# Optimization experiments

Measured on AMD Instinct MI355X. Metric: run time of the kernel, lower is better.

## Reference

```python
import jax, jax.numpy as jnp
import numpy as np

N, E, CIN, H, HEADS, B = 50000, 800000, 16, 64, 3, 64
D0 = HEADS * H            # conv1 out (heads concatenated) = 192
D1 = D0 + CIN             # x1 dim = 208
D2 = 2 * D1               # x2 dim = 416
MLP_IN = 3 * D2           # 1248
MLP_HID = MLP_IN // 2     # 624
EPS = 1e-5


def setup_inputs() -> dict:
    key = jax.random.key(0)
    ks = jax.random.split(key, 24)
    r = lambda k, s, sc=0.05: (jax.random.normal(k, s, dtype=jnp.float32) * sc)
    inp = {
        'x': jax.random.normal(ks[0], (N, CIN), dtype=jnp.float32),
        'edge_index': jax.random.randint(ks[1], (2, E), 0, N, dtype=jnp.int32),
        'edge_attr': jax.random.normal(ks[2], (E, 4), dtype=jnp.float32),
        'batch': jnp.sort(jax.random.randint(ks[3], (N,), 0, B, dtype=jnp.int32)),
        # conv1 (GeneralConv, heads=3, concat): msg/edge/self linears -> D0
        'W_msg1': r(ks[4], (CIN, D0)), 'b_msg1': jnp.zeros((D0,), jnp.float32),
        'W_edge1': r(ks[5], (4, D0)), 'b_edge1': jnp.zeros((D0,), jnp.float32),
        'W_self1': r(ks[6], (CIN, D0)), 'b_self1': jnp.zeros((D0,), jnp.float32),
        'g1': jnp.ones((D0,), jnp.float32), 'be1': jnp.zeros((D0,), jnp.float32),
        # conv2 (GeneralConv, heads=1, in==out -> identity self)
        'W_msg2': r(ks[7], (D1, D1)), 'b_msg2': jnp.zeros((D1,), jnp.float32),
        'W_edge2': r(ks[8], (4, D1)), 'b_edge2': jnp.zeros((D1,), jnp.float32),
        'g2': jnp.ones((D1,), jnp.float32), 'be2': jnp.zeros((D1,), jnp.float32),
        # MLP head
        'W_l1': r(ks[9], (MLP_IN, MLP_HID)), 'b_l1': jnp.zeros((MLP_HID,), jnp.float32),
        'alpha': jnp.asarray(0.25, jnp.float32),  # PReLU default
        'W_l2': r(ks[10], (MLP_HID, 2)), 'b_l2': jnp.zeros((2,), jnp.float32),
    }
    return inp


def _bn(h, g, b):
    m = h.mean(axis=0)
    v = h.var(axis=0)  # biased, like torch BatchNorm training mode
    return (h - m) * jax.lax.rsqrt(v + EPS) * g + b


def reference(x, edge_index, edge_attr, batch,
              W_msg1, b_msg1, W_edge1, b_edge1, W_self1, b_self1, g1, be1,
              W_msg2, b_msg2, W_edge2, b_edge2, g2, be2,
              W_l1, b_l1, alpha, W_l2, b_l2):
    src, dst = edge_index[0], edge_index[1]
    # conv1: gather -> linear msg + edge feature -> scatter-add -> + self linear
    m1 = x[src] @ W_msg1 + b_msg1 + edge_attr @ W_edge1 + b_edge1   # [E, D0]
    h1 = jax.ops.segment_sum(m1, dst, num_segments=N) + (x @ W_self1 + b_self1)
    h1 = _bn(h1, g1, be1)
    x1 = jnp.concatenate([h1, x], axis=1)                           # [N, D1]
    # conv2 (identity self-connection since in==out)
    m2 = x1[src] @ W_msg2 + b_msg2 + edge_attr @ W_edge2 + b_edge2  # [E, D1]
    h2 = jax.ops.segment_sum(m2, dst, num_segments=N) + x1
    h2 = _bn(h2, g2, be2)
    x2 = jnp.concatenate([h2, x1], axis=1)                          # [N, D2]
    # global add / mean / max pooling by graph id
    s = jax.ops.segment_sum(x2, batch, num_segments=B)
    cnt = jax.ops.segment_sum(jnp.ones((x2.shape[0], 1), x2.dtype), batch, num_segments=B)
    mean = s / jnp.maximum(cnt, 1.0)
    mx = jax.ops.segment_max(x2, batch, num_segments=B)
    pooled = jnp.concatenate([s, mx, mean], axis=1)                 # [B, 3*D2]
    # MLP head: Linear -> Dropout(0) -> PReLU -> Linear -> log_softmax
    h = pooled @ W_l1 + b_l1
    h = jnp.where(h >= 0, h, alpha * h)
    logits = h @ W_l2 + b_l2
    return jax.nn.log_softmax(logits, axis=-1)
```

## Files before the change

kernel.cpp:

```cpp
#include <hip/hip_runtime.h>

typedef __attribute__((ext_vector_type(8))) short short8;
typedef __attribute__((ext_vector_type(4))) float f32x4;
typedef unsigned short u16;
typedef unsigned int u32;

__device__ __forceinline__ u16 f2bf(float f) {
  u32 u = __float_as_uint(f);
  u = (u + 0x7fffu + ((u >> 16) & 1u)) >> 16;
  return (u16)u;
}
__device__ __forceinline__ float bf2f(u16 v) { return __uint_as_float((u32)v << 16); }
__device__ __forceinline__ void atomAddF(float* p, float v) { unsafeAtomicAdd(p, v); }
__device__ __forceinline__ void addp(float* v, u32 p) {
  v[0] += bf2f((u16)p);
  v[1] += bf2f((u16)(p >> 16));
}

__global__ void prep_k(const float* __restrict__ Wm1, const float* __restrict__ We1,
                       const float* __restrict__ Ws1, const float* __restrict__ Wm2,
                       const float* __restrict__ Wl1, const float* __restrict__ x,
                       const int* __restrict__ batch, u16* __restrict__ Wp1,
                       u16* __restrict__ Wp2, u16* __restrict__ Wp3,
                       u16* __restrict__ xbf, int* __restrict__ gstart,
                       int* __restrict__ gend, int* __restrict__ deg,
                       float* __restrict__ bns1p, float* __restrict__ bns2p, int N, int E) {
  int tid = blockIdx.x * 256 + threadIdx.x;
  if (tid < 64 * 192) {
    int k = tid / 192, n = tid % 192;
    float v = 0.f;
    if (k < 16) v = Wm1[k * 192 + n];
    else if (k < 20) v = We1[(k - 16) * 192 + n];
    else if (k < 36) v = Ws1[(k - 20) * 192 + n];
    Wp1[((k >> 3) * 192 + n) * 8 + (k & 7)] = f2bf(v);
  }
  if (tid < 224 * 208) {
    int k = tid / 208, n = tid % 208;
    float v = (k < 208) ? Wm2[k * 208 + n] : 0.f;
    Wp2[((k >> 3) * 208 + n) * 8 + (k & 7)] = f2bf(v);
  }
  if (tid < N * 8) {
    float2 p = *(const float2*)(x + (size_t)tid * 2);
    *(u32*)(xbf + (size_t)tid * 2) = (u32)f2bf(p.x) | ((u32)f2bf(p.y) << 16);
  }
  if (tid < N) {
    int b = batch[tid];
    if (tid == 0 || batch[tid - 1] != b) gstart[b] = tid;
    if (tid == N - 1 || batch[tid + 1] != b) gend[b] = tid;
    deg[tid] = 0;
  }
  if (tid < 64 * 384) bns1p[tid] = 0.f;
  if (tid < 64 * 832) bns2p[tid] = 0.f;
  if (tid < 1248 * 624) {
    int k = tid / 624, n = tid % 624;
    Wp3[((size_t)(k >> 3) * 624 + n) * 8 + (k & 7)] = f2bf(Wl1[(size_t)k * 624 + n]);
  }
}

__global__ void count_k(const int* __restrict__ ei, int* __restrict__ deg,
                        int* __restrict__ ord, int E) {
  int e = blockIdx.x * 256 + threadIdx.x;
  if (e >= E) return;
  ord[e] = atomicAdd(&deg[ei[E + e]], 1);
}

__global__ void scanA_k(const int* __restrict__ deg, int* __restrict__ bsum, int N) {
  __shared__ int sh[256];
  int t = threadIdx.x;
  int i = blockIdx.x * 256 + t;
  sh[t] = (i < N) ? deg[i] : 0;
  __syncthreads();
  for (int off = 128; off > 0; off >>= 1) {
    if (t < off) sh[t] += sh[t + off];
    __syncthreads();
  }
  if (t == 0) bsum[blockIdx.x] = sh[0];
}

__global__ void scanC_k(const int* __restrict__ deg, const int* __restrict__ bsum,
                        int* __restrict__ rowptr, int N, int nb) {
  __shared__ int sb2[256];
  __shared__ int sh[256];
  int t = threadIdx.x;
  int bv = (t < nb) ? bsum[t] : 0;
  sb2[t] = bv;
  __syncthreads();
  for (int off = 1; off < 256; off <<= 1) {
    int u = (t >= off) ? sb2[t - off] : 0;
    __syncthreads();
    sb2[t] += u;
    __syncthreads();
  }
  int bpref = (blockIdx.x == 0) ? 0 : sb2[blockIdx.x - 1];
  int i = blockIdx.x * 256 + t;
  int d = (i < N) ? deg[i] : 0;
  sh[t] = d;
  __syncthreads();
  for (int off = 1; off < 256; off <<= 1) {
    int u = (t >= off) ? sh[t - off] : 0;
    __syncthreads();
    sh[t] += u;
    __syncthreads();
  }
  int excl = sh[t] - d + bpref;
  if (i < N) {
    rowptr[i] = excl;
    if (i == N - 1) rowptr[N] = excl + d;
  }
}

__global__ void scatter_k(const int* __restrict__ ei, const float* __restrict__ ea,
                          const int* __restrict__ ord, const int* __restrict__ rowptr,
                          int4* __restrict__ se16, int E) {
  int e = blockIdx.x * 256 + threadIdx.x;
  if (e >= E) return;
  int s = ei[e], d = ei[E + e];
  float4 w = *(const float4*)(ea + (size_t)e * 4);
  int slot = rowptr[d] + ord[e];
  int4 ent;
  ent.x = s;
  ent.y = (int)((u32)f2bf(w.x) | ((u32)f2bf(w.y) << 16));
  ent.z = (int)((u32)f2bf(w.z) | ((u32)f2bf(w.w) << 16));
  ent.w = 0;
  se16[slot] = ent;
}

__global__ void __launch_bounds__(256) conv1_k(
    const int4* __restrict__ se16, const int* __restrict__ rowptr,
    const u16* __restrict__ xbf, const u16* __restrict__ Bp,
    const float* __restrict__ bm1, const float* __restrict__ be1,
    const float* __restrict__ bs1, u16* __restrict__ acc1c, u16* __restrict__ h1bf,
    float* __restrict__ bns1p, int N) {
  __shared__ __align__(16) u16 Uls[16][72];
  __shared__ float degls[16];
  int tid = threadIdx.x;
  int nl = tid >> 4, q = tid & 15;
  int n = blockIdx.x * 16 + nl;
  bool nval = n < N;
  int j0 = nval ? rowptr[n] : 0;
  int j1 = nval ? rowptr[n + 1] : 0;
  float v[20];
#pragma unroll
  for (int i = 0; i < 20; ++i) v[i] = 0.f;
  for (int j = j0 + q; j < j1; j += 16) {
    int4 p = se16[j];
    const uint4* xs = (const uint4*)(xbf + (size_t)p.x * 16);
    uint4 x0 = xs[0], x1 = xs[1];
    addp(v + 0, x0.x); addp(v + 2, x0.y); addp(v + 4, x0.z); addp(v + 6, x0.w);
    addp(v + 8, x1.x); addp(v + 10, x1.y); addp(v + 12, x1.z); addp(v + 14, x1.w);
    addp(v + 16, (u32)p.y); addp(v + 18, (u32)p.z);
  }
#pragma unroll
  for (int i = 0; i < 20; ++i) {
    v[i] += __shfl_xor(v[i], 1);
    v[i] += __shfl_xor(v[i], 2);
    v[i] += __shfl_xor(v[i], 4);
    v[i] += __shfl_xor(v[i], 8);
  }
  float degf = (float)(j1 - j0);
  const u16* xr = xbf + (size_t)n * 16;
  {
    u32 w2[2];
#pragma unroll
    for (int jj = 0; jj < 2; ++jj) {
      int t0 = q * 4 + 2 * jj, t1 = t0 + 1;
      u16 b0 = (t0 < 20) ? f2bf(v[t0]) : ((t0 < 36 && nval) ? xr[t0 - 20] : (u16)0);
      u16 b1 = (t1 < 20) ? f2bf(v[t1]) : ((t1 < 36 && nval) ? xr[t1 - 20] : (u16)0);
      w2[jj] = (u32)b0 | ((u32)b1 << 16);
    }
    *(uint2*)&Uls[nl][q * 4] = make_uint2(w2[0], w2[1]);
  }
  if (nval) {
    int t0 = q * 2, t1 = t0 + 1;
    float f0 = (t0 < 20) ? v[t0] : ((t0 == 20) ? degf : 0.f);
    float f1 = (t1 < 20) ? v[t1] : ((t1 == 20) ? degf : 0.f);
    *(u32*)(acc1c + (size_t)n * 32 + q * 2) = (u32)f2bf(f0) | ((u32)f2bf(f1) << 16);
  }
  if (q == 0) degls[nl] = degf;
  __syncthreads();
  int w = tid >> 6, lane = tid & 63, rc = lane & 15, qd = lane >> 4;
  int slice = (blockIdx.x & 63) * 384;
  for (int nt = w; nt < 12; nt += 4) {
    f32x4 acc = {0.f, 0.f, 0.f, 0.f};
#pragma unroll
    for (int kb = 0; kb < 2; ++kb) {
      short8 av = *(const short8*)&Uls[rc][kb * 32 + qd * 8];
      short8 bv = *(const short8*)(Bp + (size_t)((kb * 4 + qd) * 192 + nt * 16 + rc) * 8);
      acc = __builtin_amdgcn_mfma_f32_16x16x32_bf16(av, bv, acc, 0, 0, 0);
    }
    int col = nt * 16 + rc;
    float bb = bm1[col] + be1[col], bsv = bs1[col];
    float ps = 0.f, pq = 0.f;
#pragma unroll
    for (int r = 0; r < 4; ++r) {
      int ml = qd * 4 + r;
      int m = blockIdx.x * 16 + ml;
      float val = acc[r] + degls[ml] * bb + bsv;
      if (m < N) {
        h1bf[(size_t)m * 192 + col] = f2bf(val);
        ps += val;
        pq += val * val;
      }
    }
    ps += __shfl_xor(ps, 16); ps += __shfl_xor(ps, 32);
    pq += __shfl_xor(pq, 16); pq += __shfl_xor(pq, 32);
    if (qd == 0) {
      atomAddF(&bns1p[slice + col], ps);
      atomAddF(&bns1p[slice + 192 + col], pq);
    }
  }
}

__global__ void bnfin1_k(const float* __restrict__ bns1p, const float* __restrict__ g1,
                         const float* __restrict__ bta1, float Ninv,
                         float* __restrict__ aff1) {
  int c = threadIdx.x;
  if (c >= 192) return;
  float sm = 0.f, sq = 0.f;
  for (int k = 0; k < 64; ++k) {
    sm += bns1p[k * 384 + c];
    sq += bns1p[k * 384 + 192 + c];
  }
  float m1 = sm * Ninv;
  float var = sq * Ninv - m1 * m1;
  float s1 = g1[c] * rsqrtf(var + 1e-5f);
  aff1[c] = s1;
  aff1[192 + c] = bta1[c] - m1 * s1;
}

__global__ void __launch_bounds__(256) conv2_k(
    const int4* __restrict__ se16, const int* __restrict__ rowptr,
    const u16* __restrict__ acc1c, const u16* __restrict__ h1bf,
    const u16* __restrict__ xbf, const u16* __restrict__ Bp1, const u16* __restrict__ Bp2,
    const float* __restrict__ bm1, const float* __restrict__ be1,
    const float* __restrict__ bs1, const float* __restrict__ aff1,
    const float* __restrict__ We2, const float* __restrict__ bm2,
    const float* __restrict__ be2, float* __restrict__ bns2p,
    u16* __restrict__ h2bf, int N) {
  __shared__ __align__(16) u16 Uls[16][72];
  __shared__ __align__(16) u16 Vls[16][232];
  __shared__ float degls[16], sdegls[16], eals[16][4];
  int tid = threadIdx.x;
  int nl = tid >> 4, q = tid & 15;
  int n = blockIdx.x * 16 + nl;
  bool nval = n < N;
  int j0 = nval ? rowptr[n] : 0;
  int j1 = nval ? rowptr[n + 1] : 0;
  float v[21];
#pragma unroll
  for (int i = 0; i < 21; ++i) v[i] = 0.f;
  for (int j = j0 + q; j < j1; j += 16) {
    int s = se16[j].x;
    const uint4* cr = (const uint4*)(acc1c + (size_t)s * 32);
    uint4 c0 = cr[0], c1 = cr[1], c2 = cr[2];
    addp(v + 0, c0.x); addp(v + 2, c0.y); addp(v + 4, c0.z); addp(v + 6, c0.w);
    addp(v + 8, c1.x); addp(v + 10, c1.y); addp(v + 12, c1.z); addp(v + 14, c1.w);
    addp(v + 16, c2.x); addp(v + 18, c2.y);
    v[20] += bf2f((u16)c2.z);
  }
#pragma unroll
  for (int i = 0; i < 21; ++i) {
    v[i] += __shfl_xor(v[i], 1);
    v[i] += __shfl_xor(v[i], 2);
    v[i] += __shfl_xor(v[i], 4);
    v[i] += __shfl_xor(v[i], 8);
  }
  const u16* selfr = acc1c + (size_t)n * 32;
  {
    u32 w2[2];
#pragma unroll
    for (int jj = 0; jj < 2; ++jj) {
      int t0 = q * 4 + 2 * jj, t1 = t0 + 1;
      u16 b0 = (t0 < 20) ? f2bf(v[t0]) : ((t0 < 36 && nval) ? selfr[t0 - 20] : (u16)0);
      u16 b1 = (t1 < 20) ? f2bf(v[t1]) : ((t1 < 36 && nval) ? selfr[t1 - 20] : (u16)0);
      w2[jj] = (u32)b0 | ((u32)b1 << 16);
    }
    *(uint2*)&Uls[nl][q * 4] = make_uint2(w2[0], w2[1]);
  }
  {
    int t0 = q * 2, t1 = t0 + 1;
    u16 b0 = (t0 < 16 && nval) ? selfr[t0] : (u16)0;
    u16 b1 = (t1 < 16 && nval) ? selfr[t1] : (u16)0;
    *(u32*)&Vls[nl][192 + q * 2] = (u32)b0 | ((u32)b1 << 16);
  }
  if (q == 0) sdegls[nl] = v[20];
  if (q == 1) degls[nl] = nval ? bf2f(selfr[20]) : 0.f;
  if (q == 2) {
#pragma unroll
    for (int k = 0; k < 4; ++k) eals[nl][k] = nval ? bf2f(selfr[16 + k]) : 0.f;
  }
  __syncthreads();
  int w = tid >> 6, lane = tid & 63, rc = lane & 15, qd = lane >> 4;
  for (int nt = w; nt < 12; nt += 4) {
    f32x4 acc = {0.f, 0.f, 0.f, 0.f};
#pragma unroll
    for (int kb = 0; kb < 2; ++kb) {
      short8 av = *(const short8*)&Uls[rc][kb * 32 + qd * 8];
      short8 bv = *(const short8*)(Bp1 + (size_t)((kb * 4 + qd) * 192 + nt * 16 + rc) * 8);
      acc = __builtin_amdgcn_mfma_f32_16x16x32_bf16(av, bv, acc, 0, 0, 0);
    }
    int col = nt * 16 + rc;
    float s1 = aff1[col], t1 = aff1[192 + col];
    float bb = bm1[col] + be1[col], bsv = bs1[col];
#pragma unroll
    for (int r = 0; r < 4; ++r) {
      int ml = qd * 4 + r;
      float qv = acc[r] + sdegls[ml] * bb + degls[ml] * bsv;
      Vls[ml][col] = f2bf(qv * s1 + degls[ml] * t1);
    }
  }
  __syncthreads();
  int slice = (blockIdx.x & 63) * 832;
  for (int nt = w; nt < 13; nt += 4) {
    f32x4 acc = {0.f, 0.f, 0.f, 0.f};
#pragma unroll
    for (int kb = 0; kb < 7; ++kb) {
      short8 av = *(const short8*)&Vls[rc][kb * 32 + qd * 8];
      short8 bv = *(const short8*)(Bp2 + (size_t)((kb * 4 + qd) * 208 + nt * 16 + rc) * 8);
      acc = __builtin_amdgcn_mfma_f32_16x16x32_bf16(av, bv, acc, 0, 0, 0);
    }
    int col = nt * 16 + rc;
    float w0 = We2[col], w1 = We2[208 + col], w2 = We2[416 + col], w3 = We2[624 + col];
    float bb2 = bm2[col] + be2[col];
    bool c192 = col < 192;
    float s1 = c192 ? aff1[col] : 0.f;
    float t1 = c192 ? aff1[192 + col] : 0.f;
    float ps = 0.f, pq = 0.f;
#pragma unroll
    for (int r = 0; r < 4; ++r) {
      int ml = qd * 4 + r;
      int m = blockIdx.x * 16 + ml;
      bool mv = m < N;
      float x1 = 0.f;
      if (mv) {
        x1 = c192 ? (bf2f(h1bf[(size_t)m * 192 + col]) * s1 + t1)
                  : bf2f(xbf[(size_t)m * 16 + (col - 192)]);
      }
      float val = acc[r] + eals[ml][0] * w0 + eals[ml][1] * w1 + eals[ml][2] * w2 +
                  eals[ml][3] * w3 + degls[ml] * bb2 + x1;
      if (mv) {
        h2bf[(size_t)m * 208 + col] = f2bf(val);
        ps += val;
        pq += val * val;
      }
    }
    ps += __shfl_xor(ps, 16); ps += __shfl_xor(ps, 32);
    pq += __shfl_xor(pq, 16); pq += __shfl_xor(pq, 32);
    if (qd == 0) {
      atomAddF(&bns2p[slice + col], ps);
      atomAddF(&bns2p[slice + 416 + col], pq);
    }
  }
}

__global__ void bnfin2_k(const float* __restrict__ bns2p, const float* __restrict__ aff1,
                         const float* __restrict__ g2, const float* __restrict__ bta2,
                         float Ninv, float* __restrict__ aff) {
  int f = blockIdx.x * 256 + threadIdx.x;
  if (f >= 416) return;
  float sc, sh;
  if (f < 208) {
    float sm = 0.f, sq = 0.f;
    for (int k = 0; k < 64; ++k) {
      sm += bns2p[k * 832 + f];
      sq += bns2p[k * 832 + 416 + f];
    }
    float m2 = sm * Ninv;
    float var = sq * Ninv - m2 * m2;
    sc = g2[f] * rsqrtf(var + 1e-5f);
    sh = bta2[f] - m2 * sc;
  } else if (f < 400) {
    sc = aff1[f - 208];
    sh = aff1[192 + (f - 208)];
  } else {
    sc = 1.f;
    sh = 0.f;
  }
  aff[f] = sc;
  aff[416 + f] = sh;
}

__global__ void pool_k(const u16* __restrict__ h2bf, const u16* __restrict__ h1bf,
                       const u16* __restrict__ xbf, const float* __restrict__ aff,
                       const int* __restrict__ gstart, const int* __restrict__ gend,
                       float* __restrict__ psp, float* __restrict__ pmp) {
  int b = blockIdx.x, sub = blockIdx.y;
  int t = threadIdx.x;
  if (t >= 208) return;
  int s0 = gstart[b], e0 = gend[b];
  int cnt = (s0 <= e0) ? e0 - s0 + 1 : 0;
  int per = (cnt + 15) >> 4;
  int n0 = s0 + sub * per;
  int n1 = min(n0 + per, s0 + cnt);
  int f = 2 * t;
  const u16* src;
  int stride;
  if (f < 208) { src = h2bf + f; stride = 208; }
  else if (f < 400) { src = h1bf + (f - 208); stride = 192; }
  else { src = xbf + (f - 400); stride = 16; }
  float sc0 = aff[f], sc1 = aff[f + 1];
  float sh0 = aff[416 + f], sh1 = aff[417 + f];
  float s0f = 0.f, s1f = 0.f, m0f = -3.4e38f, m1f = -3.4e38f;
  for (int n = n0; n < n1; ++n) {
    u32 p = *(const u32*)(src + (size_t)n * stride);
    float v0 = bf2f((u16)p) * sc0 + sh0;
    float v1 = bf2f((u16)(p >> 16)) * sc1 + sh1;
    s0f += v0; s1f += v1;
    m0f = fmaxf(m0f, v0); m1f = fmaxf(m1f, v1);
  }
  size_t idx = ((size_t)(b * 16 + sub)) * 416 + f;
  *(float2*)(psp + idx) = make_float2(s0f, s1f);
  *(float2*)(pmp + idx) = make_float2(m0f, m1f);
}

__global__ void pooledprep_k(const float* __restrict__ psp, const float* __restrict__ pmp,
                             const int* __restrict__ gstart, const int* __restrict__ gend,
                             u16* __restrict__ Apool) {
  int b = blockIdx.x, t = threadIdx.x;
  int cnt = gend[b] - gstart[b] + 1;
  float inv = 1.f / (float)max(cnt, 1);
  for (int f = t; f < 416; f += 256) {
    float s = 0.f, m = -3.4e38f;
    for (int k = 0; k < 16; ++k) {
      size_t idx = ((size_t)(b * 16 + k)) * 416 + f;
      s += psp[idx];
      m = fmaxf(m, pmp[idx]);
    }
    u16* row = Apool + (size_t)b * 1248;
    row[f] = f2bf(s);
    row[416 + f] = f2bf((cnt > 0) ? m : 0.f);
    row[832 + f] = f2bf(s * inv);
  }
}

__global__ void mlpgemm_k(const u16* __restrict__ A, const u16* __restrict__ Bp,
                          const float* __restrict__ b1, const float* __restrict__ al,
                          float* __restrict__ hid) {
  int lane = threadIdx.x;
  int mt = blockIdx.x, nt = blockIdx.y;
  int rc = lane & 15, qd = lane >> 4;
  f32x4 acc = {0.f, 0.f, 0.f, 0.f};
  const u16* Ap = A + (size_t)(mt * 16 + rc) * 1248 + qd * 8;
  const u16* Bq = Bp + (size_t)(qd * 624 + nt * 16 + rc) * 8;
  for (int kb = 0; kb < 39; ++kb) {
    short8 av = *(const short8*)(Ap + kb * 32);
    short8 bv = *(const short8*)(Bq + (size_t)kb * 4 * 624 * 8);
    acc = __builtin_amdgcn_mfma_f32_16x16x32_bf16(av, bv, acc, 0, 0, 0);
  }
  int col = nt * 16 + rc;
  float bb = b1[col], alpha = al[0];
  int m0 = mt * 16 + qd * 4;
#pragma unroll
  for (int r = 0; r < 4; ++r) {
    float v = acc[r] + bb;
    hid[(size_t)(m0 + r) * 624 + col] = (v >= 0.f) ? v : alpha * v;
  }
}

__global__ void head_k(const float* __restrict__ hid, const float* __restrict__ W2,
                       const float* __restrict__ b2, float* __restrict__ out) {
  int b = blockIdx.x, t = threadIdx.x;
  float p0 = 0.f, p1 = 0.f;
  for (int k = t; k < 624; k += 64) {
    float h = hid[(size_t)b * 624 + k];
    p0 += h * W2[k * 2];
    p1 += h * W2[k * 2 + 1];
  }
#pragma unroll
  for (int off = 32; off > 0; off >>= 1) {
    p0 += __shfl_down(p0, off);
    p1 += __shfl_down(p1, off);
  }
  if (t == 0) {
    float l0 = p0 + b2[0], l1 = p1 + b2[1];
    float m = fmaxf(l0, l1);
    float lse = m + logf(expf(l0 - m) + expf(l1 - m));
    out[b * 2] = l0 - lse;
    out[b * 2 + 1] = l1 - lse;
  }
}

extern "C" void kernel_launch(void* const* d_in, const int* in_sizes, int n_in,
                              void* d_out, int out_size, void* d_ws, size_t ws_size,
                              hipStream_t stream) {
  const float* x = (const float*)d_in[0];
  const int* ei = (const int*)d_in[1];
  const float* ea = (const float*)d_in[2];
  const int* batch = (const int*)d_in[3];
  const float* Wm1 = (const float*)d_in[4];
  const float* bm1 = (const float*)d_in[5];
  const float* We1 = (const float*)d_in[6];
  const float* be1 = (const float*)d_in[7];
  const float* Ws1 = (const float*)d_in[8];
  const float* bs1 = (const float*)d_in[9];
  const float* g1 = (const float*)d_in[10];
  const float* bta1 = (const float*)d_in[11];
  const float* Wm2 = (const float*)d_in[12];
  const float* bm2 = (const float*)d_in[13];
  const float* We2 = (const float*)d_in[14];
  const float* be2 = (const float*)d_in[15];
  const float* g2 = (const float*)d_in[16];
  const float* bta2 = (const float*)d_in[17];
  const float* Wl1 = (const float*)d_in[18];
  const float* bl1 = (const float*)d_in[19];
  const float* alpha = (const float*)d_in[20];
  const float* Wl2 = (const float*)d_in[21];
  const float* bl2 = (const float*)d_in[22];
  float* out = (float*)d_out;

  const int N = in_sizes[3];
  const int E = in_sizes[2] / 4;
  const int nb = (N + 255) / 256;
  const float Ninv = 1.f / (float)N;

  float* ws = (float*)d_ws;
  size_t o = 0;
  u16* acc1c = (u16*)(ws + o); o += (size_t)N * 16;
  u16* h2bf = (u16*)(ws + o);  o += (size_t)N * 104;
  u16* h1bf = (u16*)(ws + o);  o += (size_t)N * 96;
  u16* xbf = (u16*)(ws + o);   o += (size_t)N * 8;
  u16* Wp1 = (u16*)(ws + o);   o += 6144;
  u16* Wp2 = (u16*)(ws + o);   o += 23296;
  u16* Wp3 = (u16*)(ws + o);   o += 389376;
  u16* Apool = (u16*)(ws + o); o += 39936;
  float* hid = ws + o;    o += 64 * 624;
  float* bns1p = ws + o;  o += 64 * 384;
  float* bns2p = ws + o;  o += 64 * 832;
  float* aff1 = ws + o;   o += 384;
  float* aff = ws + o;    o += 832;
  float* psp = ws + o;    o += (size_t)64 * 16 * 416;
  float* pmp = ws + o;    o += (size_t)64 * 16 * 416;
  int* gstart = (int*)(ws + o); o += 64;
  int* gend = (int*)(ws + o);   o += 64;
  int* deg = (int*)(ws + o);    o += N;
  int* rowptr = (int*)(ws + o); o += N + 1;
  int* ord = (int*)(ws + o);    o += E;
  int* bsum = (int*)(ws + o);   o += 256;
  o = (o + 3) & ~(size_t)3;
  int4* se16 = (int4*)(ws + o); o += (size_t)4 * E;

  const int gconv = (N + 15) / 16;
  prep_k<<<(E + 255) / 256, 256, 0, stream>>>(Wm1, We1, Ws1, Wm2, Wl1, x, batch, Wp1, Wp2,
                                              Wp3, xbf, gstart, gend, deg, bns1p, bns2p,
                                              N, E);
  count_k<<<(E + 255) / 256, 256, 0, stream>>>(ei, deg, ord, E);
  scanA_k<<<nb, 256, 0, stream>>>(deg, bsum, N);
  scanC_k<<<nb, 256, 0, stream>>>(deg, bsum, rowptr, N, nb);
  scatter_k<<<(E + 255) / 256, 256, 0, stream>>>(ei, ea, ord, rowptr, se16, E);
  conv1_k<<<gconv, 256, 0, stream>>>(se16, rowptr, xbf, Wp1, bm1, be1, bs1, acc1c, h1bf,
                                     bns1p, N);
  bnfin1_k<<<1, 256, 0, stream>>>(bns1p, g1, bta1, Ninv, aff1);
  conv2_k<<<gconv, 256, 0, stream>>>(se16, rowptr, acc1c, h1bf, xbf, Wp1, Wp2, bm1, be1,
                                     bs1, aff1, We2, bm2, be2, bns2p, h2bf, N);
  bnfin2_k<<<2, 256, 0, stream>>>(bns2p, aff1, g2, bta2, Ninv, aff);
  pool_k<<<dim3(64, 16), 256, 0, stream>>>(h2bf, h1bf, xbf, aff, gstart, gend, psp, pmp);
  pooledprep_k<<<64, 256, 0, stream>>>(psp, pmp, gstart, gend, Apool);
  mlpgemm_k<<<dim3(4, 39), 64, 0, stream>>>(Apool, Wp3, bl1, alpha, hid);
  head_k<<<64, 64, 0, stream>>>(hid, Wl2, bl2, out);
}
```

Measured before the change: 304.9 us.

## Two-pass bucketed edge scatter, merge degree count into prep, memset zeroing

Moves the degree-count atomics into the prep kernel and zeroes deg, the bucket counters and the BN partial buffers with one hipMemsetAsync instead of inside prep. Replaces the direct random scatter of CSR entries with two passes: edges are first binned into 32K-slot buckets by destination slot with shared-memory histograms, and then written to their final slots from bucket order. This should make the final writes more localized and cut scattered write traffic. In exchange it adds an extra kernel, a bucket buffer and a second read/write of all edges.

```diff
diff --git a/kernel.cpp b/kernel.cpp
--- a/kernel.cpp
+++ b/kernel.cpp
@@ -20,11 +20,11 @@
 __global__ void prep_k(const float* __restrict__ Wm1, const float* __restrict__ We1,
                        const float* __restrict__ Ws1, const float* __restrict__ Wm2,
                        const float* __restrict__ Wl1, const float* __restrict__ x,
-                       const int* __restrict__ batch, u16* __restrict__ Wp1,
-                       u16* __restrict__ Wp2, u16* __restrict__ Wp3,
+                       const int* __restrict__ batch, const int* __restrict__ ei,
+                       u16* __restrict__ Wp1, u16* __restrict__ Wp2, u16* __restrict__ Wp3,
                        u16* __restrict__ xbf, int* __restrict__ gstart,
                        int* __restrict__ gend, int* __restrict__ deg,
-                       float* __restrict__ bns1p, float* __restrict__ bns2p, int N, int E) {
+                       int* __restrict__ ord, int N, int E) {
   int tid = blockIdx.x * 256 + threadIdx.x;
   if (tid < 64 * 192) {
     int k = tid / 192, n = tid % 192;
@@ -47,21 +47,12 @@
     int b = batch[tid];
     if (tid == 0 || batch[tid - 1] != b) gstart[b] = tid;
     if (tid == N - 1 || batch[tid + 1] != b) gend[b] = tid;
-    deg[tid] = 0;
-  }
-  if (tid < 64 * 384) bns1p[tid] = 0.f;
-  if (tid < 64 * 832) bns2p[tid] = 0.f;
+  }
   if (tid < 1248 * 624) {
     int k = tid / 624, n = tid % 624;
     Wp3[((size_t)(k >> 3) * 624 + n) * 8 + (k & 7)] = f2bf(Wl1[(size_t)k * 624 + n]);
   }
-}
-
-__global__ void count_k(const int* __restrict__ ei, int* __restrict__ deg,
-                        int* __restrict__ ord, int E) {
-  int e = blockIdx.x * 256 + threadIdx.x;
-  if (e >= E) return;
-  ord[e] = atomicAdd(&deg[ei[E + e]], 1);
+  if (tid < E) ord[tid] = atomicAdd(&deg[ei[E + tid]], 1);
 }
 
 __global__ void scanA_k(const int* __restrict__ deg, int* __restrict__ bsum, int N) {
@@ -109,20 +100,42 @@
   }
 }
 
-__global__ void scatter_k(const int* __restrict__ ei, const float* __restrict__ ea,
-                          const int* __restrict__ ord, const int* __restrict__ rowptr,
-                          int4* __restrict__ se16, int E) {
-  int e = blockIdx.x * 256 + threadIdx.x;
-  if (e >= E) return;
-  int s = ei[e], d = ei[E + e];
-  float4 w = *(const float4*)(ea + (size_t)e * 4);
-  int slot = rowptr[d] + ord[e];
-  int4 ent;
-  ent.x = s;
-  ent.y = (int)((u32)f2bf(w.x) | ((u32)f2bf(w.y) << 16));
-  ent.z = (int)((u32)f2bf(w.z) | ((u32)f2bf(w.w) << 16));
-  ent.w = 0;
-  se16[slot] = ent;
+__global__ void bucket_k(const int* __restrict__ ei, const float* __restrict__ ea,
+                         const int* __restrict__ ord, const int* __restrict__ rowptr,
+                         int* __restrict__ gcnt, int4* __restrict__ bkt, int E) {
+  __shared__ int hcnt[32];
+  __shared__ int hbase[32];
+  int tid = threadIdx.x;
+  int e = blockIdx.x * 256 + tid;
+  if (tid < 32) hcnt[tid] = 0;
+  __syncthreads();
+  bool valid = e < E;
+  int slot = 0, b = 0, myofs = 0, s = 0;
+  u32 p0 = 0, p1 = 0;
+  if (valid) {
+    s = ei[e];
+    int d = ei[E + e];
+    float4 w = *(const float4*)(ea + (size_t)e * 4);
+    p0 = (u32)f2bf(w.x) | ((u32)f2bf(w.y) << 16);
+    p1 = (u32)f2bf(w.z) | ((u32)f2bf(w.w) << 16);
+    slot = rowptr[d] + ord[e];
+    b = slot >> 15;
+    myofs = atomicAdd(&hcnt[b], 1);
+  }
+  __syncthreads();
+  if (tid < 32) hbase[tid] = hcnt[tid] ? atomicAdd(&gcnt[tid], hcnt[tid]) : 0;
+  __syncthreads();
+  if (valid) {
+    int pos = (b << 15) + hbase[b] + myofs;
+    bkt[pos] = make_int4(slot, s, (int)p0, (int)p1);
+  }
+}
+
+__global__ void order_k(const int4* __restrict__ bkt, int4* __restrict__ se16, int E) {
+  int p = blockIdx.x * 256 + threadIdx.x;
+  if (p >= E) return;
+  int4 ent = bkt[p];
+  se16[ent.x] = make_int4(ent.y, ent.z, ent.w, 0);
 }
 
 __global__ void __launch_bounds__(256) conv1_k(
@@ -512,6 +525,7 @@
   const int E = in_sizes[2] / 4;
   const int nb = (N + 255) / 256;
   const float Ninv = 1.f / (float)N;
+  const int NBK = (E + 32767) >> 15;
 
   float* ws = (float*)d_ws;
   size_t o = 0;
@@ -524,29 +538,33 @@
   u16* Wp3 = (u16*)(ws + o);   o += 389376;
   u16* Apool = (u16*)(ws + o); o += 39936;
   float* hid = ws + o;    o += 64 * 624;
+  int* deg = (int*)(ws + o);    o += N;
+  int* gcnt = (int*)(ws + o);   o += 32;
   float* bns1p = ws + o;  o += 64 * 384;
   float* bns2p = ws + o;  o += 64 * 832;
+  size_t zbytes = ((size_t)N + 32 + 64 * 384 + 64 * 832) * sizeof(float);
   float* aff1 = ws + o;   o += 384;
   float* aff = ws + o;    o += 832;
   float* psp = ws + o;    o += (size_t)64 * 16 * 416;
   float* pmp = ws + o;    o += (size_t)64 * 16 * 416;
   int* gstart = (int*)(ws + o); o += 64;
   int* gend = (int*)(ws + o);   o += 64;
-  int* deg = (int*)(ws + o);    o += N;
   int* rowptr = (int*)(ws + o); o += N + 1;
   int* ord = (int*)(ws + o);    o += E;
   int* bsum = (int*)(ws + o);   o += 256;
   o = (o + 3) & ~(size_t)3;
   int4* se16 = (int4*)(ws + o); o += (size_t)4 * E;
+  int4* bkt = (int4*)(ws + o);  o += (size_t)4 * ((size_t)NBK << 15);
 
   const int gconv = (N + 15) / 16;
-  prep_k<<<(E + 255) / 256, 256, 0, stream>>>(Wm1, We1, Ws1, Wm2, Wl1, x, batch, Wp1, Wp2,
-                                              Wp3, xbf, gstart, gend, deg, bns1p, bns2p,
-                                              N, E);
-  count_k<<<(E + 255) / 256, 256, 0, stream>>>(ei, deg, ord, E);
+  const int ge = (E + 255) / 256;
+  hipMemsetAsync(deg, 0, zbytes, stream);
+  prep_k<<<ge, 256, 0, stream>>>(Wm1, We1, Ws1, Wm2, Wl1, x, batch, ei, Wp1, Wp2, Wp3, xbf,
+                                 gstart, gend, deg, ord, N, E);
   scanA_k<<<nb, 256, 0, stream>>>(deg, bsum, N);
   scanC_k<<<nb, 256, 0, stream>>>(deg, bsum, rowptr, N, nb);
-  scatter_k<<<(E + 255) / 256, 256, 0, stream>>>(ei, ea, ord, rowptr, se16, E);
+  bucket_k<<<ge, 256, 0, stream>>>(ei, ea, ord, rowptr, gcnt, bkt, E);
+  order_k<<<ge, 256, 0, stream>>>(bkt, se16, E);
   conv1_k<<<gconv, 256, 0, stream>>>(se16, rowptr, xbf, Wp1, bm1, be1, bs1, acc1c, h1bf,
                                      bns1p, N);
   bnfin1_k<<<1, 256, 0, stream>>>(bns1p, g1, bta1, Ninv, aff1);
```

New measurement: 341.1 us. 1.12x slower.
